# Optimization experiments

Hardware: AMD Instinct MI355X
Metric: run time of the kernel (lower is better)

Reference implementation:

```python
import math
import jax, jax.numpy as jnp
import numpy as np

B, S, D = 1, 2048, 4096
H, KVH, HD = 32, 8, 128  # head_dim = D // H; n_rep = H // KVH = 4
MAXB, MAXS = 1, 2048
ROPE_THETA = 10000.0


def setup_inputs() -> dict:
    key = jax.random.key(0)
    ks = jax.random.split(key, 6)
    x = jax.random.normal(ks[0], (B, S, D), dtype=jnp.float32)
    sc = 0.02
    wq = jax.random.normal(ks[1], (D, H * HD), dtype=jnp.float32) * sc
    wk = jax.random.normal(ks[2], (D, KVH * HD), dtype=jnp.float32) * sc
    wv = jax.random.normal(ks[3], (D, KVH * HD), dtype=jnp.float32) * sc
    wo = jax.random.normal(ks[4], (H * HD, D), dtype=jnp.float32) * sc
    # rotary phases: freqs_cis[t, j] = exp(i * t * theta^(-2j/hd))
    inv_freq = 1.0 / (ROPE_THETA ** (jnp.arange(0, HD, 2, dtype=jnp.float32) / HD))
    ang = jnp.arange(S, dtype=jnp.float32)[:, None] * inv_freq[None, :]  # [S, HD//2]
    freqs_cos = jnp.cos(ang)
    freqs_sin = jnp.sin(ang)
    # causal additive mask over the cache window (start_pos=0 prefill)
    mask = jnp.where(jnp.triu(jnp.ones((S, S), dtype=bool), k=1), -1e9, 0.0).astype(jnp.float32)
    cache_k = jnp.zeros((MAXB, MAXS, KVH, HD), dtype=jnp.float32)
    cache_v = jnp.zeros((MAXB, MAXS, KVH, HD), dtype=jnp.float32)
    return {"x": x, "wq": wq, "wk": wk, "wv": wv, "wo": wo,
            "freqs_cos": freqs_cos, "freqs_sin": freqs_sin, "mask": mask,
            "cache_k": cache_k, "cache_v": cache_v, "start_pos": 0}


def _apply_rope(t, cos, sin):
    # t: [B, S, h, HD]; cos/sin: [S, HD//2]
    te, to = t[..., ::2], t[..., 1::2]
    cos = cos[None, :, None, :]
    sin = sin[None, :, None, :]
    out = jnp.stack([te * cos - to * sin, to * cos + te * sin], axis=-1)
    return out.reshape(t.shape)


def _repeat_kv(t, n_rep):
    # faithful to source: rep axis inserted before kv-head axis
    bs, slen, n_kv, hd = t.shape
    if n_rep == 1:
        return t
    return jnp.repeat(t[:, :, None, :, :], n_rep, axis=2).reshape(bs, slen, n_kv * n_rep, hd)


def reference(x, wq, wk, wv, wo, freqs_cos, freqs_sin, mask, cache_k, cache_v, start_pos):
    bsz, seqlen, _ = x.shape
    n_rep = H // KVH
    xq = (x @ wq).reshape(bsz, seqlen, H, HD)
    xk = (x @ wk).reshape(bsz, seqlen, KVH, HD)
    xv = (x @ wv).reshape(bsz, seqlen, KVH, HD)
    xq = _apply_rope(xq, freqs_cos, freqs_sin)
    xk = _apply_rope(xk, freqs_cos, freqs_sin)
    # KV-cache append
    cache_k = cache_k.at[:bsz, start_pos:start_pos + seqlen].set(xk)
    cache_v = cache_v.at[:bsz, start_pos:start_pos + seqlen].set(xv)
    keys = _repeat_kv(cache_k[:bsz, :start_pos + seqlen], n_rep)    # [B, T, H, HD]
    values = _repeat_kv(cache_v[:bsz, :start_pos + seqlen], n_rep)  # [B, T, H, HD]
    scores = jnp.einsum('bqhd,bkhd->bhqk', xq, keys) / math.sqrt(HD)
    scores = scores + mask[None, None, :, :]
    probs = jax.nn.softmax(scores, axis=-1)
    out = jnp.einsum('bhqk,bkhd->bqhd', probs, values).reshape(bsz, seqlen, H * HD)
    return out @ wo
```

## Files before the change

### kernel.cpp

```cpp
#include <hip/hip_runtime.h>
#include <stdint.h>


using bf16x8 = __attribute__((ext_vector_type(8))) short;
using f32x4  = __attribute__((ext_vector_type(4))) float;
using s16x4  = __attribute__((ext_vector_type(4))) short;

__device__ __forceinline__ short f2bf(float f) {
    union { float f; unsigned u; } v; v.f = f;
    unsigned r = v.u + 0x7fffu + ((v.u >> 16) & 1u);
    return (short)(r >> 16);
}
__device__ __forceinline__ float bf2f(short s) {
    union { unsigned u; float f; } v; v.u = ((unsigned)(unsigned short)s) << 16;
    return v.f;
}

#define GLL16(gp, lp)                                                          \
    __builtin_amdgcn_global_load_lds(                                          \
        (const __attribute__((address_space(1))) void*)(gp),                   \
        (__attribute__((address_space(3))) void*)(lp), 16, 0, 0)

__global__ __launch_bounds__(256) void cvt_f32_bf16(const float* __restrict__ x,
                                                    short* __restrict__ y, int n) {
    int i = (blockIdx.x * 256 + threadIdx.x) * 4;
    if (i >= n) return;
    f32x4 v = *(const f32x4*)(x + i);
    s16x4 o;
    o.x = f2bf(v.x); o.y = f2bf(v.y); o.z = f2bf(v.z); o.w = f2bf(v.w);
    *(s16x4*)(y + i) = o;
}

__global__ __launch_bounds__(256) void transpose_w4(const float* __restrict__ wq,
                                                    const float* __restrict__ wk,
                                                    const float* __restrict__ wv,
                                                    const float* __restrict__ wo,
                                                    short* __restrict__ wqkvT,
                                                    short* __restrict__ woT) {
    __shared__ float t[64][65];
    int by = blockIdx.y;
    const float* W; short* WT; int N;
    if (by < 64)      { W = wq; WT = wqkvT;                         N = 4096; }
    else if (by < 80) { W = wk; WT = wqkvT + (size_t)4096 * 4096;   N = 1024; by -= 64; }
    else if (by < 96) { W = wv; WT = wqkvT + (size_t)5120 * 4096;   N = 1024; by -= 80; }
    else              { W = wo; WT = woT;                           N = 4096; by -= 96; }
    const int n0 = by * 64, k0 = blockIdx.x * 64;
    const int tx = threadIdx.x & 63, ty = threadIdx.x >> 6;
#pragma unroll
    for (int i = 0; i < 16; i++) {
        int r = ty * 16 + i;
        t[r][tx] = W[(size_t)(k0 + r) * N + n0 + tx];
    }
    __syncthreads();
#pragma unroll
    for (int it = 0; it < 4; it++) {
        int nr = it * 16 + (threadIdx.x >> 4);
        int c  = threadIdx.x & 15;
        s16x4 o;
#pragma unroll
        for (int j = 0; j < 4; j++) o[j] = f2bf(t[c * 4 + j][nr]);
        *(s16x4*)&WT[(size_t)(n0 + nr) * 4096 + k0 + c * 4] = o;
    }
}

__global__ __launch_bounds__(256) void transpose_bf16(const short* __restrict__ A,
                                                      short* __restrict__ AT,
                                                      int R, int C, int lda) {
    __shared__ short t[32][33];
    int c0 = blockIdx.x * 32, r0 = blockIdx.y * 32;
    int tx = threadIdx.x, ty = threadIdx.y;
#pragma unroll
    for (int i = 0; i < 32; i += 8)
        t[ty + i][tx] = A[(size_t)(r0 + ty + i) * lda + c0 + tx];
    __syncthreads();
#pragma unroll
    for (int i = 0; i < 32; i += 8)
        AT[(size_t)(c0 + ty + i) * R + r0 + tx] = t[tx][ty + i];
}

__global__ __launch_bounds__(256) void gemm_bf16(const short* __restrict__ A,
                                                 const short* __restrict__ BT,
                                                 float* __restrict__ Cf,
                                                 short* __restrict__ Cb,
                                                 short* __restrict__ Cb2,
                                                 int M, int N, int K,
                                                 int split, int ld1, int ld2) {
    __shared__ short As[128 * 32];
    __shared__ short Bs[128 * 32];
    const int tid  = threadIdx.x;
    const int wave = tid >> 6, lane = tid & 63;
    const int lrow = lane & 15, quad = lane >> 4, lk8 = quad * 8;
    const int bm = blockIdx.y * 128, bn = blockIdx.x * 128;
    const int wm = (wave >> 1) * 64, wn = (wave & 1) * 64;

    f32x4 acc[4][4];
#pragma unroll
    for (int i = 0; i < 4; i++)
#pragma unroll
        for (int j = 0; j < 4; j++) acc[i][j] = (f32x4){0.f, 0.f, 0.f, 0.f};

    for (int k0 = 0; k0 < K; k0 += 32) {
        __syncthreads();
#pragma unroll
        for (int s = 0; s < 2; s++) {
            int idx = tid * 8 + s * 2048;
            int row = idx >> 5, col = idx & 31;
            GLL16(A  + (size_t)(bm + row) * K + k0 + col, &As[idx]);
            GLL16(BT + (size_t)(bn + row) * K + k0 + col, &Bs[idx]);
        }
        __syncthreads();
        bf16x8 af[4], bfr[4];
#pragma unroll
        for (int i = 0; i < 4; i++) af[i]  = *(const bf16x8*)&As[(wm + i * 16 + lrow) * 32 + lk8];
#pragma unroll
        for (int j = 0; j < 4; j++) bfr[j] = *(const bf16x8*)&Bs[(wn + j * 16 + lrow) * 32 + lk8];
#pragma unroll
        for (int i = 0; i < 4; i++)
#pragma unroll
            for (int j = 0; j < 4; j++)
                acc[i][j] = __builtin_amdgcn_mfma_f32_16x16x32_bf16(af[i], bfr[j], acc[i][j], 0, 0, 0);
    }

    short* Co;
    int ldc, ncol0;
    if (bn < split) { Co = Cb;  ldc = ld1; ncol0 = 0;     }
    else            { Co = Cb2; ldc = ld2; ncol0 = split; }

#pragma unroll
    for (int i = 0; i < 4; i++)
#pragma unroll
        for (int j = 0; j < 4; j++)
#pragma unroll
            for (int r = 0; r < 4; r++) {
                int m = bm + wm + i * 16 + quad * 4 + r;
                int n = bn + wn + j * 16 + lrow;
                float v = acc[i][j][r];
                if (Cf) Cf[(size_t)m * N + n] = v;
                else    Co[(size_t)m * ldc + (n - ncol0)] = f2bf(v);
            }
}

__global__ __launch_bounds__(256) void rope_kernel(short* __restrict__ q,
                                                   short* __restrict__ kv,
                                                   const float* __restrict__ fc,
                                                   const float* __restrict__ fs) {
    int s = blockIdx.x, t = threadIdx.x;
#pragma unroll
    for (int p = t; p < 2048; p += 256) {
        int i = p & 63;
        float c = fc[s * 64 + i], sn = fs[s * 64 + i];
        int base = s * 4096 + 2 * p;
        float e = bf2f(q[base]), o = bf2f(q[base + 1]);
        q[base]     = f2bf(e * c - o * sn);
        q[base + 1] = f2bf(o * c + e * sn);
    }
#pragma unroll
    for (int p = t; p < 512; p += 256) {
        int i = p & 63;
        float c = fc[s * 64 + i], sn = fs[s * 64 + i];
        int base = s * 2048 + 2 * p;
        float e = bf2f(kv[base]), o = bf2f(kv[base + 1]);
        kv[base]     = f2bf(e * c - o * sn);
        kv[base + 1] = f2bf(o * c + e * sn);
    }
}

#define KSLD 136
#define VSLD 40
__global__ __launch_bounds__(256) void attn_kernel(const short* __restrict__ Q,
                                                   const short* __restrict__ KV,
                                                   const short* __restrict__ VT,
                                                   short* __restrict__ AO) {
    const int qb = 63 - blockIdx.x;
    const int kvh = blockIdx.y;
    const int wave = threadIdx.x >> 6, lane = threadIdx.x & 63;
    const int lrow = lane & 15, quad = lane >> 4, lk8 = quad * 8;
    const int h = wave * 8 + kvh;
    const int q0 = qb * 32;

    __shared__ short Ks[32 * KSLD];
    __shared__ short Vs[128 * VSLD];
    __shared__ short Pw[4][2][16 * 32];

    bf16x8 aq[2][4];
#pragma unroll
    for (int rs = 0; rs < 2; rs++) {
        const short* qrow = Q + (size_t)(q0 + rs * 16 + lrow) * 4096 + h * 128;
#pragma unroll
        for (int f = 0; f < 4; f++) aq[rs][f] = *(const bf16x8*)(qrow + f * 32 + lk8);
    }

    f32x4 o_acc[2][8];
#pragma unroll
    for (int rs = 0; rs < 2; rs++)
#pragma unroll
        for (int d = 0; d < 8; d++) o_acc[rs][d] = (f32x4){0.f, 0.f, 0.f, 0.f};
    float l_part[2][4];
#pragma unroll
    for (int rs = 0; rs < 2; rs++)
#pragma unroll
        for (int r = 0; r < 4; r++) l_part[rs][r] = 0.f;

    const int nkt = qb + 1;
    const float sc = 0.08838834764831845f;

    for (int kt = 0; kt < nkt; kt++) {
        __syncthreads();
#pragma unroll
        for (int c = 0; c < 2; c++) {
            int idx = (threadIdx.x + c * 256) * 8;
            int key = idx >> 7, d = idx & 127;
            *(bf16x8*)&Ks[key * KSLD + d] =
                *(const bf16x8*)(KV + (size_t)(kt * 32 + key) * 2048 + kvh * 128 + d);
            int dr = idx >> 5, kc = idx & 31;
            *(bf16x8*)&Vs[dr * VSLD + kc] =
                *(const bf16x8*)(VT + (size_t)(kvh * 128 + dr) * 2048 + kt * 32 + kc);
        }
        __syncthreads();

        f32x4 s0[2], s1[2];
#pragma unroll
        for (int rs = 0; rs < 2; rs++) { s0[rs] = (f32x4){0.f,0.f,0.f,0.f}; s1[rs] = s0[rs]; }
#pragma unroll
        for (int f = 0; f < 4; f++) {
            bf16x8 b0 = *(const bf16x8*)&Ks[(lrow)      * KSLD + f * 32 + lk8];
            bf16x8 b1 = *(const bf16x8*)&Ks[(16 + lrow) * KSLD + f * 32 + lk8];
#pragma unroll
            for (int rs = 0; rs < 2; rs++) {
                s0[rs] = __builtin_amdgcn_mfma_f32_16x16x32_bf16(aq[rs][f], b0, s0[rs], 0, 0, 0);
                s1[rs] = __builtin_amdgcn_mfma_f32_16x16x32_bf16(aq[rs][f], b1, s1[rs], 0, 0, 0);
            }
        }

        int keyg0 = kt * 32 + lrow, keyg1 = keyg0 + 16;
#pragma unroll
        for (int rs = 0; rs < 2; rs++)
#pragma unroll
            for (int r = 0; r < 4; r++) {
                int qg = q0 + rs * 16 + quad * 4 + r;
                float p0 = (keyg0 > qg) ? 0.f : __expf(s0[rs][r] * sc);
                float p1 = (keyg1 > qg) ? 0.f : __expf(s1[rs][r] * sc);
                l_part[rs][r] += p0 + p1;
                Pw[wave][rs][(quad * 4 + r) * 32 + lrow]      = f2bf(p0);
                Pw[wave][rs][(quad * 4 + r) * 32 + 16 + lrow] = f2bf(p1);
            }

#pragma unroll
        for (int rs = 0; rs < 2; rs++) {
            bf16x8 ap = *(const bf16x8*)&Pw[wave][rs][lrow * 32 + lk8];
#pragma unroll
            for (int dt = 0; dt < 8; dt++) {
                bf16x8 bv = *(const bf16x8*)&Vs[(dt * 16 + lrow) * VSLD + lk8];
                o_acc[rs][dt] = __builtin_amdgcn_mfma_f32_16x16x32_bf16(ap, bv, o_acc[rs][dt], 0, 0, 0);
            }
        }
    }

#pragma unroll
    for (int rs = 0; rs < 2; rs++)
#pragma unroll
        for (int r = 0; r < 4; r++) {
            float l = l_part[rs][r];
#pragma unroll
            for (int off = 1; off < 16; off <<= 1) l += __shfl_xor(l, off, 64);
            float inv = 1.f / l;
#pragma unroll
            for (int dt = 0; dt < 8; dt++) {
                int qg = q0 + rs * 16 + quad * 4 + r;
                AO[(size_t)qg * 4096 + h * 128 + dt * 16 + lrow] =
                    f2bf(o_acc[rs][dt][r] * inv);
            }
        }
}

extern "C" void kernel_launch(void* const* d_in, const int* in_sizes, int n_in,
                              void* d_out, int out_size, void* d_ws, size_t ws_size,
                              hipStream_t stream) {
    (void)in_sizes; (void)n_in; (void)out_size; (void)ws_size;
    const float* x  = (const float*)d_in[0];
    const float* wq = (const float*)d_in[1];
    const float* wk = (const float*)d_in[2];
    const float* wv = (const float*)d_in[3];
    const float* wo = (const float*)d_in[4];
    const float* fc = (const float*)d_in[5];
    const float* fs = (const float*)d_in[6];
    float* out = (float*)d_out;

    char* ws = (char*)d_ws;
    size_t off = 0;
    auto carve = [&](size_t bytes) { char* p = ws + off; off = (off + bytes + 255) & ~(size_t)255; return p; };
    short* xb     = (short*)carve(2048u * 4096u * 2);
    short* wqkvT  = (short*)carve(6144u * 4096u * 2);
    short* woT    = (short*)carve(4096u * 4096u * 2);
    short* qb     = (short*)carve(2048u * 4096u * 2);
    short* kvb    = (short*)carve(2048u * 2048u * 2);
    short* vtb    = (short*)carve(1024u * 2048u * 2);
    short* aob    = xb;

    dim3 tb(32, 8);
    cvt_f32_bf16<<<8192, 256, 0, stream>>>(x, xb, 2048 * 4096);
    transpose_w4<<<dim3(64, 160), 256, 0, stream>>>(wq, wk, wv, wo, wqkvT, woT);

    gemm_bf16<<<dim3(48, 16), 256, 0, stream>>>(xb, wqkvT, nullptr, qb, kvb,
                                                2048, 6144, 4096, 4096, 4096, 2048);

    rope_kernel<<<2048, 256, 0, stream>>>(qb, kvb, fc, fs);
    transpose_bf16<<<dim3(32, 64), tb, 0, stream>>>(kvb + 1024, vtb, 2048, 1024, 2048);

    attn_kernel<<<dim3(64, 8), 256, 0, stream>>>(qb, kvb, vtb, aob);

    gemm_bf16<<<dim3(32, 16), 256, 0, stream>>>(aob, woT, out, nullptr, nullptr,
                                                2048, 4096, 4096, 4096, 4096, 4096);
}
```

Baseline: 606.7 us.

## Write V transposed from QKV GEMM epilogue and load K/V fragments directly in attention

The QKV GEMM epilogue now writes the V columns directly in transposed layout, which removes the separate transpose_bf16 kernel and the K-only buffer's stride change. The attention kernel drops LDS staging of K and V tiles and the two block-wide barriers per key tile. Each wave instead loads its MFMA fragments straight from global memory, and the P scratch buffer gets padding to reduce bank conflicts. The risk is that all four waves now load the same K/V data redundantly from global/L2 and the loads are less coalesced, so the global-load latency is no longer hidden behind shared staging.

```diff
diff --git a/kernel.cpp b/kernel.cpp
--- a/kernel.cpp
+++ b/kernel.cpp
@@ -63,28 +63,15 @@
     }
 }
 
-__global__ __launch_bounds__(256) void transpose_bf16(const short* __restrict__ A,
-                                                      short* __restrict__ AT,
-                                                      int R, int C, int lda) {
-    __shared__ short t[32][33];
-    int c0 = blockIdx.x * 32, r0 = blockIdx.y * 32;
-    int tx = threadIdx.x, ty = threadIdx.y;
-#pragma unroll
-    for (int i = 0; i < 32; i += 8)
-        t[ty + i][tx] = A[(size_t)(r0 + ty + i) * lda + c0 + tx];
-    __syncthreads();
-#pragma unroll
-    for (int i = 0; i < 32; i += 8)
-        AT[(size_t)(c0 + ty + i) * R + r0 + tx] = t[tx][ty + i];
-}
-
 __global__ __launch_bounds__(256) void gemm_bf16(const short* __restrict__ A,
                                                  const short* __restrict__ BT,
                                                  float* __restrict__ Cf,
                                                  short* __restrict__ Cb,
                                                  short* __restrict__ Cb2,
+                                                 short* __restrict__ Cv,
                                                  int M, int N, int K,
-                                                 int split, int ld1, int ld2) {
+                                                 int split, int ld1, int ld2,
+                                                 int vsplit) {
     __shared__ short As[128 * 32];
     __shared__ short Bs[128 * 32];
     const int tid  = threadIdx.x;
@@ -121,11 +108,37 @@
                 acc[i][j] = __builtin_amdgcn_mfma_f32_16x16x32_bf16(af[i], bfr[j], acc[i][j], 0, 0, 0);
     }
 
+    if (Cf) {
+#pragma unroll
+        for (int i = 0; i < 4; i++)
+#pragma unroll
+            for (int j = 0; j < 4; j++)
+#pragma unroll
+                for (int r = 0; r < 4; r++) {
+                    int m = bm + wm + i * 16 + quad * 4 + r;
+                    int n = bn + wn + j * 16 + lrow;
+                    Cf[(size_t)m * N + n] = acc[i][j][r];
+                }
+        return;
+    }
+    if (bn >= vsplit) {
+#pragma unroll
+        for (int i = 0; i < 4; i++)
+#pragma unroll
+            for (int j = 0; j < 4; j++) {
+                int c = bn + wn + j * 16 + lrow - vsplit;
+                int m = bm + wm + i * 16 + quad * 4;
+                s16x4 o;
+#pragma unroll
+                for (int r = 0; r < 4; r++) o[r] = f2bf(acc[i][j][r]);
+                *(s16x4*)&Cv[(size_t)c * M + m] = o;
+            }
+        return;
+    }
     short* Co;
     int ldc, ncol0;
     if (bn < split) { Co = Cb;  ldc = ld1; ncol0 = 0;     }
     else            { Co = Cb2; ldc = ld2; ncol0 = split; }
-
 #pragma unroll
     for (int i = 0; i < 4; i++)
 #pragma unroll
@@ -134,9 +147,7 @@
             for (int r = 0; r < 4; r++) {
                 int m = bm + wm + i * 16 + quad * 4 + r;
                 int n = bn + wn + j * 16 + lrow;
-                float v = acc[i][j][r];
-                if (Cf) Cf[(size_t)m * N + n] = v;
-                else    Co[(size_t)m * ldc + (n - ncol0)] = f2bf(v);
+                Co[(size_t)m * ldc + (n - ncol0)] = f2bf(acc[i][j][r]);
             }
 }
 
@@ -158,17 +169,16 @@
     for (int p = t; p < 512; p += 256) {
         int i = p & 63;
         float c = fc[s * 64 + i], sn = fs[s * 64 + i];
-        int base = s * 2048 + 2 * p;
+        int base = s * 1024 + 2 * p;
         float e = bf2f(kv[base]), o = bf2f(kv[base + 1]);
         kv[base]     = f2bf(e * c - o * sn);
         kv[base + 1] = f2bf(o * c + e * sn);
     }
 }
 
-#define KSLD 136
-#define VSLD 40
+#define PSLD 36
 __global__ __launch_bounds__(256) void attn_kernel(const short* __restrict__ Q,
-                                                   const short* __restrict__ KV,
+                                                   const short* __restrict__ K,
                                                    const short* __restrict__ VT,
                                                    short* __restrict__ AO) {
     const int qb = 63 - blockIdx.x;
@@ -178,9 +188,7 @@
     const int h = wave * 8 + kvh;
     const int q0 = qb * 32;
 
-    __shared__ short Ks[32 * KSLD];
-    __shared__ short Vs[128 * VSLD];
-    __shared__ short Pw[4][2][16 * 32];
+    __shared__ short Pw[4][2][16 * PSLD];
 
     bf16x8 aq[2][4];
 #pragma unroll
@@ -203,28 +211,23 @@
 
     const int nkt = qb + 1;
     const float sc = 0.08838834764831845f;
+    const short* vbase = VT + (size_t)(kvh * 128 + lrow) * 2048 + lk8;
 
     for (int kt = 0; kt < nkt; kt++) {
-        __syncthreads();
-#pragma unroll
-        for (int c = 0; c < 2; c++) {
-            int idx = (threadIdx.x + c * 256) * 8;
-            int key = idx >> 7, d = idx & 127;
-            *(bf16x8*)&Ks[key * KSLD + d] =
-                *(const bf16x8*)(KV + (size_t)(kt * 32 + key) * 2048 + kvh * 128 + d);
-            int dr = idx >> 5, kc = idx & 31;
-            *(bf16x8*)&Vs[dr * VSLD + kc] =
-                *(const bf16x8*)(VT + (size_t)(kvh * 128 + dr) * 2048 + kt * 32 + kc);
-        }
-        __syncthreads();
+        const short* kbase = K + (size_t)(kt * 32 + lrow) * 1024 + kvh * 128 + lk8;
+
+        bf16x8 bv[8];
+#pragma unroll
+        for (int dt = 0; dt < 8; dt++)
+            bv[dt] = *(const bf16x8*)(vbase + (size_t)(dt * 16) * 2048 + kt * 32);
 
         f32x4 s0[2], s1[2];
 #pragma unroll
         for (int rs = 0; rs < 2; rs++) { s0[rs] = (f32x4){0.f,0.f,0.f,0.f}; s1[rs] = s0[rs]; }
 #pragma unroll
         for (int f = 0; f < 4; f++) {
-            bf16x8 b0 = *(const bf16x8*)&Ks[(lrow)      * KSLD + f * 32 + lk8];
-            bf16x8 b1 = *(const bf16x8*)&Ks[(16 + lrow) * KSLD + f * 32 + lk8];
+            bf16x8 b0 = *(const bf16x8*)(kbase + f * 32);
+            bf16x8 b1 = *(const bf16x8*)(kbase + (size_t)16 * 1024 + f * 32);
 #pragma unroll
             for (int rs = 0; rs < 2; rs++) {
                 s0[rs] = __builtin_amdgcn_mfma_f32_16x16x32_bf16(aq[rs][f], b0, s0[rs], 0, 0, 0);
@@ -241,18 +244,16 @@
                 float p0 = (keyg0 > qg) ? 0.f : __expf(s0[rs][r] * sc);
                 float p1 = (keyg1 > qg) ? 0.f : __expf(s1[rs][r] * sc);
                 l_part[rs][r] += p0 + p1;
-                Pw[wave][rs][(quad * 4 + r) * 32 + lrow]      = f2bf(p0);
-                Pw[wave][rs][(quad * 4 + r) * 32 + 16 + lrow] = f2bf(p1);
+                Pw[wave][rs][(quad * 4 + r) * PSLD + lrow]      = f2bf(p0);
+                Pw[wave][rs][(quad * 4 + r) * PSLD + 16 + lrow] = f2bf(p1);
             }
 
 #pragma unroll
         for (int rs = 0; rs < 2; rs++) {
-            bf16x8 ap = *(const bf16x8*)&Pw[wave][rs][lrow * 32 + lk8];
-#pragma unroll
-            for (int dt = 0; dt < 8; dt++) {
-                bf16x8 bv = *(const bf16x8*)&Vs[(dt * 16 + lrow) * VSLD + lk8];
-                o_acc[rs][dt] = __builtin_amdgcn_mfma_f32_16x16x32_bf16(ap, bv, o_acc[rs][dt], 0, 0, 0);
-            }
+            bf16x8 ap = *(const bf16x8*)&Pw[wave][rs][lrow * PSLD + lk8];
+#pragma unroll
+            for (int dt = 0; dt < 8; dt++)
+                o_acc[rs][dt] = __builtin_amdgcn_mfma_f32_16x16x32_bf16(ap, bv[dt], o_acc[rs][dt], 0, 0, 0);
         }
     }
 
@@ -293,22 +294,22 @@
     short* wqkvT  = (short*)carve(6144u * 4096u * 2);
     short* woT    = (short*)carve(4096u * 4096u * 2);
     short* qb     = (short*)carve(2048u * 4096u * 2);
-    short* kvb    = (short*)carve(2048u * 2048u * 2);
+    short* kvb    = (short*)carve(2048u * 1024u * 2);
     short* vtb    = (short*)carve(1024u * 2048u * 2);
     short* aob    = xb;
 
-    dim3 tb(32, 8);
     cvt_f32_bf16<<<8192, 256, 0, stream>>>(x, xb, 2048 * 4096);
     transpose_w4<<<dim3(64, 160), 256, 0, stream>>>(wq, wk, wv, wo, wqkvT, woT);
 
-    gemm_bf16<<<dim3(48, 16), 256, 0, stream>>>(xb, wqkvT, nullptr, qb, kvb,
-                                                2048, 6144, 4096, 4096, 4096, 2048);
+    gemm_bf16<<<dim3(48, 16), 256, 0, stream>>>(xb, wqkvT, nullptr, qb, kvb, vtb,
+                                                2048, 6144, 4096,
+                                                4096, 4096, 1024, 5120);
 
     rope_kernel<<<2048, 256, 0, stream>>>(qb, kvb, fc, fs);
-    transpose_bf16<<<dim3(32, 64), tb, 0, stream>>>(kvb + 1024, vtb, 2048, 1024, 2048);
 
     attn_kernel<<<dim3(64, 8), 256, 0, stream>>>(qb, kvb, vtb, aob);
 
-    gemm_bf16<<<dim3(32, 16), 256, 0, stream>>>(aob, woT, out, nullptr, nullptr,
-                                                2048, 4096, 4096, 4096, 4096, 4096);
-}
+    gemm_bf16<<<dim3(32, 16), 256, 0, stream>>>(aob, woT, out, nullptr, nullptr, nullptr,
+                                                2048, 4096, 4096,
+                                                4096, 4096, 4096, 1 << 30);
+}
```

After: 732.2 us. 20.7% more time.
